# Performance work log

Hardware: AMD Instinct MI355X
Metric: run time of the kernel (lower is better)

Reference implementation:

```python
import jax, jax.numpy as jnp
import numpy as np
from jax import lax

IMAGE_SIZE = 224
BLUR_SIGMA = 4.0   # PIL GaussianBlur(radius=4) ~ sigma 4
BLUR_RADIUS = 8    # kernel support = 2*radius+1 = 17


def _gaussian_blur(img):
    # img: [1,1,H,W]; separable gaussian applied as a single 2D depthwise conv
    x = jnp.arange(-BLUR_RADIUS, BLUR_RADIUS + 1, dtype=img.dtype)
    k1 = jnp.exp(-0.5 * (x / BLUR_SIGMA) ** 2)
    k1 = k1 / k1.sum()
    k2 = jnp.outer(k1, k1)[None, None]  # [1,1,K,K]
    pad = jnp.pad(img, ((0, 0), (0, 0), (BLUR_RADIUS, BLUR_RADIUS), (BLUR_RADIUS, BLUR_RADIUS)), mode='reflect')
    return lax.conv_general_dilated(pad, k2, (1, 1), 'VALID',
                                    dimension_numbers=('NCHW', 'OIHW', 'NCHW'))


def _level_map(lib, fmap, idx):
    # lib: [N,C,H,W], fmap: [1,C,H,W], idx: [k]
    nearest = lib[idx]                                     # gather -> [k,C,H,W]
    d = jnp.sqrt(jnp.sum((nearest - fmap) ** 2, axis=1))   # L2 over channels -> [k,H,W]
    smin = jnp.min(d, axis=0)                              # min over k neighbors -> [H,W]
    # bilinear upsample (half-pixel centers == torch align_corners=False)
    up = jax.image.resize(smin, (IMAGE_SIZE, IMAGE_SIZE), method='bilinear')
    return up[None, None]                                  # [1,1,224,224]


def reference(z, z_lib, fmap0, fmap1, fmap2, lib0, lib1, lib2, k):
    # image-level kNN score
    dist = jnp.sqrt(jnp.sum((z_lib - z[None, :]) ** 2, axis=1))  # [N]
    neg_vals, idx = lax.top_k(-dist, k)                          # k smallest distances
    z_score = jnp.mean(-neg_vals)
    # pixel-level anomaly map: per-level min distance over the k nearest images
    s_map = (_level_map(lib0, fmap0, idx)
             + _level_map(lib1, fmap1, idx)
             + _level_map(lib2, fmap2, idx))
    return (z_score, _gaussian_blur(s_map))


def setup_inputs() -> dict:
    key = jax.random.key(0)
    ks = jax.random.split(key, 8)
    N = 128
    return {
        'z': jax.random.normal(ks[0], (1024,), dtype=jnp.float32),
        'z_lib': jax.random.normal(ks[1], (N, 1024), dtype=jnp.float32),
        'fmap0': jax.random.normal(ks[2], (1, 256, 56, 56), dtype=jnp.float32),
        'fmap1': jax.random.normal(ks[3], (1, 512, 28, 28), dtype=jnp.float32),
        'fmap2': jax.random.normal(ks[4], (1, 1024, 14, 14), dtype=jnp.float32),
        'lib0': jax.random.normal(ks[5], (N, 256, 56, 56), dtype=jnp.float32),
        'lib1': jax.random.normal(ks[6], (N, 512, 28, 28), dtype=jnp.float32),
        'lib2': jax.random.normal(ks[7], (N, 1024, 14, 14), dtype=jnp.float32),
        'k': 50,
    }
```

## Files before the change

kernel.cpp:

```cpp
#include <hip/hip_runtime.h>
#include <math.h>

#define NLIB 128
#define INFBITS 0x7F800000u

typedef float f32x4 __attribute__((ext_vector_type(4)));

static __device__ __forceinline__ int iclamp(int v, int lo, int hi) {
    return v < lo ? lo : (v > hi ? hi : v);
}

__global__ __launch_bounds__(256)
void row_dist_kernel(const float* __restrict__ z, const float* __restrict__ z_lib,
                     float* __restrict__ dist2) {
    const int n = blockIdx.x;
    const int tid = threadIdx.x, wave = tid >> 6, lane = tid & 63;
    const f32x4 a = ((const f32x4*)(z_lib + (size_t)n * 1024))[tid];
    const f32x4 b = ((const f32x4*)z)[tid];
    f32x4 d = a - b;
    f32x4 s = d * d;
    float acc = s[0] + s[1] + s[2] + s[3];
    for (int off = 32; off > 0; off >>= 1) acc += __shfl_down(acc, off, 64);
    __shared__ float ws4[4];
    if (lane == 0) ws4[wave] = acc;
    __syncthreads();
    if (tid == 0) dist2[n] = ws4[0] + ws4[1] + ws4[2] + ws4[3];
}

__global__ __launch_bounds__(128)
void select_kernel(const float* __restrict__ dist2, const int* __restrict__ kp,
                   float* __restrict__ zscore, int* __restrict__ idx,
                   unsigned* __restrict__ sb0, unsigned* __restrict__ sb1,
                   unsigned* __restrict__ sb2) {
    __shared__ float d[NLIB];
    __shared__ float contrib[NLIB];
    const int tid = threadIdx.x;
    d[tid] = dist2[tid];
    for (int i = tid; i < 3136; i += 128) sb0[i] = INFBITS;
    for (int i = tid; i < 784;  i += 128) sb1[i] = INFBITS;
    for (int i = tid; i < 196;  i += 128) sb2[i] = INFBITS;
    __syncthreads();
    const int k = *kp;
    const float dd = d[tid];
    int rank = 0;
#pragma unroll 8
    for (int m = 0; m < NLIB; ++m) {
        const float dm = d[m];
        rank += (dm < dd || (dm == dd && m < tid)) ? 1 : 0;
    }
    if (rank < k) idx[rank] = tid;
    contrib[tid] = (rank < k) ? sqrtf(dd) : 0.f;
    __syncthreads();
    if (tid == 0) {
        float s = 0.f;
        for (int m = 0; m < NLIB; ++m) s += contrib[m];
        zscore[0] = s / (float)k;
    }
}

template <int C, int NQ, int QT>
static __device__ __forceinline__ void dist_min_level(const float* __restrict__ lib,
                                                      const float* __restrict__ fmap,
                                                      int img, int qt,
                                                      unsigned* __restrict__ sb,
                                                      f32x4* __restrict__ part) {
    constexpr int G  = 256 / QT;
    constexpr int CW = C / G;
    const int tid = threadIdx.x;
    const int ql  = tid & (QT - 1);
    const int g   = tid / QT;
    const int q   = qt * QT + ql;
    const int qc  = q < NQ ? q : NQ - 1;
    const f32x4* __restrict__ lp = (const f32x4*)lib + ((size_t)img * C + g * CW) * NQ + qc;
    const f32x4* __restrict__ fp = (const f32x4*)fmap + ((size_t)g * CW) * NQ + qc;
    f32x4 acc = {};
#pragma unroll 8
    for (int c = 0; c < CW; ++c) {
        f32x4 a = lp[(size_t)c * NQ];
        f32x4 f = fp[(size_t)c * NQ];
        f32x4 d = a - f;
        acc += d * d;
    }
    part[tid] = acc;
    __syncthreads();
    if (tid < QT && q < NQ) {
        f32x4 s = part[tid];
#pragma unroll
        for (int gg = 1; gg < G; ++gg) s += part[gg * QT + tid];
        atomicMin(sb + q * 4 + 0, __float_as_uint(s[0]));
        atomicMin(sb + q * 4 + 1, __float_as_uint(s[1]));
        atomicMin(sb + q * 4 + 2, __float_as_uint(s[2]));
        atomicMin(sb + q * 4 + 3, __float_as_uint(s[3]));
    }
}

__global__ __launch_bounds__(256)
void dist_min_kernel(const float* __restrict__ lib0, const float* __restrict__ fmap0,
                     const float* __restrict__ lib1, const float* __restrict__ fmap1,
                     const float* __restrict__ lib2, const float* __restrict__ fmap2,
                     const int* __restrict__ kp, const int* __restrict__ idx,
                     unsigned* __restrict__ sb0, unsigned* __restrict__ sb1,
                     unsigned* __restrict__ sb2) {
    __shared__ f32x4 part[256];
    const int n = blockIdx.y;
    if (n >= *kp) return;
    const int t = blockIdx.x;
    const int img = idx[n];
    if (t < 13)      dist_min_level<256, 784, 64>(lib0, fmap0, img, t, sb0, part);
    else if (t < 20) dist_min_level<512, 196, 32>(lib1, fmap1, img, t - 13, sb1, part);
    else             dist_min_level<1024, 49, 16>(lib2, fmap2, img, t - 20, sb2, part);
}

static __device__ __forceinline__ void samp(int o, float inv_f, int sz, int& i0, int& i1,
                                            float& fr) {
    float c  = (o + 0.5f) * inv_f - 0.5f;
    float fl = floorf(c);
    fr = c - fl;
    int i = (int)fl;
    i0 = iclamp(i, 0, sz - 1);
    i1 = iclamp(i + 1, 0, sz - 1);
}

static __device__ __forceinline__ float ldsq(const unsigned* __restrict__ sb, int w, int y, int x) {
    return sqrtf(__uint_as_float(sb[y * w + x]));
}

static __device__ __forceinline__ float bilerp_sq(const unsigned* __restrict__ sb, int w,
                                                  int y0, int y1, int x0, int x1,
                                                  float fy, float fx) {
    float a = ldsq(sb, w, y0, x0), b = ldsq(sb, w, y0, x1);
    float c = ldsq(sb, w, y1, x0), d = ldsq(sb, w, y1, x1);
    float top = a + (b - a) * fx;
    float bot = c + (d - c) * fx;
    return top + (bot - top) * fy;
}

static __device__ __forceinline__ int reflect224(int i) {
    if (i < 0) i = -i;
    if (i > 223) i = 446 - i;
    return i;
}

static __device__ __forceinline__ void gauss_w(float* w) {
    float tot = 0.f;
#pragma unroll
    for (int j = 0; j < 17; ++j) {
        float t = (j - 8) * 0.25f;
        w[j] = expf(-0.5f * t * t);
        tot += w[j];
    }
    float inv = 1.f / tot;
#pragma unroll
    for (int j = 0; j < 17; ++j) w[j] *= inv;
}

__global__ __launch_bounds__(256)
void up_blurh_kernel(const unsigned* __restrict__ sb0, const unsigned* __restrict__ sb1,
                     const unsigned* __restrict__ sb2, float* __restrict__ tmp) {
    __shared__ float row[224];
    const int y = blockIdx.x, x = threadIdx.x;
    int y0, y1, x0, x1; float fy, fx;
    if (x < 224) {
        float v = 0.f;
        samp(y, 0.25f, 56, y0, y1, fy);   samp(x, 0.25f, 56, x0, x1, fx);
        v += bilerp_sq(sb0, 56, y0, y1, x0, x1, fy, fx);
        samp(y, 0.125f, 28, y0, y1, fy);  samp(x, 0.125f, 28, x0, x1, fx);
        v += bilerp_sq(sb1, 28, y0, y1, x0, x1, fy, fx);
        samp(y, 0.0625f, 14, y0, y1, fy); samp(x, 0.0625f, 14, x0, x1, fx);
        v += bilerp_sq(sb2, 14, y0, y1, x0, x1, fy, fx);
        row[x] = v;
    }
    __syncthreads();
    if (x < 224) {
        float w[17];
        gauss_w(w);
        float acc = 0.f;
#pragma unroll
        for (int j = 0; j < 17; ++j) acc += w[j] * row[reflect224(x + j - 8)];
        tmp[y * 224 + x] = acc;
    }
}

__global__ __launch_bounds__(256)
void blur_v_kernel(const float* __restrict__ in, float* __restrict__ out) {
    const int i = blockIdx.x * blockDim.x + threadIdx.x;
    if (i >= 224 * 224) return;
    const int y = i / 224, x = i % 224;
    float w[17];
    gauss_w(w);
    float acc = 0.f;
#pragma unroll
    for (int j = 0; j < 17; ++j) acc += w[j] * in[reflect224(y + j - 8) * 224 + x];
    out[i] = acc;
}

extern "C" void kernel_launch(void* const* d_in, const int* in_sizes, int n_in,
                              void* d_out, int out_size, void* d_ws, size_t ws_size,
                              hipStream_t stream) {
    const float* z     = (const float*)d_in[0];
    const float* z_lib = (const float*)d_in[1];
    const float* fmap0 = (const float*)d_in[2];
    const float* fmap1 = (const float*)d_in[3];
    const float* fmap2 = (const float*)d_in[4];
    const float* lib0  = (const float*)d_in[5];
    const float* lib1  = (const float*)d_in[6];
    const float* lib2  = (const float*)d_in[7];
    const int*   kp    = (const int*)d_in[8];
    float* out = (float*)d_out;

    constexpr size_t OFF_IDX   = 0;
    constexpr size_t OFF_DIST2 = 1024;
    constexpr size_t OFF_SB0   = 2048;
    constexpr size_t OFF_SB1   = 16384;
    constexpr size_t OFF_SB2   = 20480;
    constexpr size_t OFF_TMP   = 24576;

    char* ws = (char*)d_ws;
    int*      idx   = (int*)(ws + OFF_IDX);
    float*    dist2 = (float*)(ws + OFF_DIST2);
    unsigned* sb0   = (unsigned*)(ws + OFF_SB0);
    unsigned* sb1   = (unsigned*)(ws + OFF_SB1);
    unsigned* sb2   = (unsigned*)(ws + OFF_SB2);
    float*    tmp   = (float*)(ws + OFF_TMP);

    row_dist_kernel<<<dim3(NLIB), dim3(256), 0, stream>>>(z, z_lib, dist2);
    select_kernel<<<dim3(1), dim3(128), 0, stream>>>(dist2, kp, out, idx, sb0, sb1, sb2);
    dist_min_kernel<<<dim3(24, NLIB), dim3(256), 0, stream>>>(
        lib0, fmap0, lib1, fmap1, lib2, fmap2, kp, idx, sb0, sb1, sb2);
    up_blurh_kernel<<<dim3(224), dim3(256), 0, stream>>>(sb0, sb1, sb2, tmp);
    blur_v_kernel<<<dim3(196), dim3(256), 0, stream>>>(tmp, out + 1);
}
```

Before: 82.40 us.

## Process two images per block, fuse upsample and blur, fold init

```diff
diff --git a/kernel.cpp b/kernel.cpp
--- a/kernel.cpp
+++ b/kernel.cpp
@@ -12,9 +12,15 @@
 
 __global__ __launch_bounds__(256)
 void row_dist_kernel(const float* __restrict__ z, const float* __restrict__ z_lib,
-                     float* __restrict__ dist2) {
+                     float* __restrict__ dist2, unsigned* __restrict__ sb0,
+                     unsigned* __restrict__ sb1, unsigned* __restrict__ sb2) {
     const int n = blockIdx.x;
     const int tid = threadIdx.x, wave = tid >> 6, lane = tid & 63;
+    const int gid = n * 256 + tid;
+    if (gid < 3136)      sb0[gid] = INFBITS;
+    else if (gid < 3920) sb1[gid - 3136] = INFBITS;
+    else if (gid < 4116) sb2[gid - 3920] = INFBITS;
+
     const f32x4 a = ((const f32x4*)(z_lib + (size_t)n * 1024))[tid];
     const f32x4 b = ((const f32x4*)z)[tid];
     f32x4 d = a - b;
@@ -29,16 +35,11 @@
 
 __global__ __launch_bounds__(128)
 void select_kernel(const float* __restrict__ dist2, const int* __restrict__ kp,
-                   float* __restrict__ zscore, int* __restrict__ idx,
-                   unsigned* __restrict__ sb0, unsigned* __restrict__ sb1,
-                   unsigned* __restrict__ sb2) {
+                   float* __restrict__ zscore, int* __restrict__ idx) {
     __shared__ float d[NLIB];
     __shared__ float contrib[NLIB];
     const int tid = threadIdx.x;
     d[tid] = dist2[tid];
-    for (int i = tid; i < 3136; i += 128) sb0[i] = INFBITS;
-    for (int i = tid; i < 784;  i += 128) sb1[i] = INFBITS;
-    for (int i = tid; i < 196;  i += 128) sb2[i] = INFBITS;
     __syncthreads();
     const int k = *kp;
     const float dd = d[tid];
@@ -61,9 +62,10 @@
 template <int C, int NQ, int QT>
 static __device__ __forceinline__ void dist_min_level(const float* __restrict__ lib,
                                                       const float* __restrict__ fmap,
-                                                      int img, int qt,
+                                                      int img0, int img1, int qt,
                                                       unsigned* __restrict__ sb,
-                                                      f32x4* __restrict__ part) {
+                                                      f32x4* __restrict__ partA,
+                                                      f32x4* __restrict__ partB) {
     constexpr int G  = 256 / QT;
     constexpr int CW = C / G;
     const int tid = threadIdx.x;
@@ -71,26 +73,39 @@
     const int g   = tid / QT;
     const int q   = qt * QT + ql;
     const int qc  = q < NQ ? q : NQ - 1;
-    const f32x4* __restrict__ lp = (const f32x4*)lib + ((size_t)img * C + g * CW) * NQ + qc;
-    const f32x4* __restrict__ fp = (const f32x4*)fmap + ((size_t)g * CW) * NQ + qc;
-    f32x4 acc = {};
-#pragma unroll 8
+    const f32x4* __restrict__ lp0 = (const f32x4*)lib + ((size_t)img0 * C + g * CW) * NQ + qc;
+    const f32x4* __restrict__ lp1 = (const f32x4*)lib + ((size_t)img1 * C + g * CW) * NQ + qc;
+    const f32x4* __restrict__ fp  = (const f32x4*)fmap + ((size_t)g * CW) * NQ + qc;
+    f32x4 acc0 = {}, acc1 = {};
+#pragma unroll 4
     for (int c = 0; c < CW; ++c) {
-        f32x4 a = lp[(size_t)c * NQ];
-        f32x4 f = fp[(size_t)c * NQ];
-        f32x4 d = a - f;
-        acc += d * d;
-    }
-    part[tid] = acc;
+        f32x4 f  = fp[(size_t)c * NQ];
+        f32x4 a0 = __builtin_nontemporal_load(lp0 + (size_t)c * NQ);
+        f32x4 a1 = __builtin_nontemporal_load(lp1 + (size_t)c * NQ);
+        f32x4 d0 = a0 - f;
+        f32x4 d1 = a1 - f;
+        acc0 += d0 * d0;
+        acc1 += d1 * d1;
+    }
+    partA[tid] = acc0;
+    partB[tid] = acc1;
     __syncthreads();
     if (tid < QT && q < NQ) {
-        f32x4 s = part[tid];
-#pragma unroll
-        for (int gg = 1; gg < G; ++gg) s += part[gg * QT + tid];
-        atomicMin(sb + q * 4 + 0, __float_as_uint(s[0]));
-        atomicMin(sb + q * 4 + 1, __float_as_uint(s[1]));
-        atomicMin(sb + q * 4 + 2, __float_as_uint(s[2]));
-        atomicMin(sb + q * 4 + 3, __float_as_uint(s[3]));
+        f32x4 s0 = partA[tid];
+        f32x4 s1 = partB[tid];
+#pragma unroll
+        for (int gg = 1; gg < G; ++gg) {
+            s0 += partA[gg * QT + tid];
+            s1 += partB[gg * QT + tid];
+        }
+        atomicMin(sb + q * 4 + 0, __float_as_uint(s0[0]));
+        atomicMin(sb + q * 4 + 1, __float_as_uint(s0[1]));
+        atomicMin(sb + q * 4 + 2, __float_as_uint(s0[2]));
+        atomicMin(sb + q * 4 + 3, __float_as_uint(s0[3]));
+        atomicMin(sb + q * 4 + 0, __float_as_uint(s1[0]));
+        atomicMin(sb + q * 4 + 1, __float_as_uint(s1[1]));
+        atomicMin(sb + q * 4 + 2, __float_as_uint(s1[2]));
+        atomicMin(sb + q * 4 + 3, __float_as_uint(s1[3]));
     }
 }
 
@@ -101,14 +116,17 @@
                      const int* __restrict__ kp, const int* __restrict__ idx,
                      unsigned* __restrict__ sb0, unsigned* __restrict__ sb1,
                      unsigned* __restrict__ sb2) {
-    __shared__ f32x4 part[256];
-    const int n = blockIdx.y;
-    if (n >= *kp) return;
+    __shared__ f32x4 partA[256];
+    __shared__ f32x4 partB[256];
+    const int k = *kp;
+    const int n0 = blockIdx.y * 2;
+    if (n0 >= k) return;
+    const int n1 = (n0 + 1 < k) ? n0 + 1 : k - 1;
     const int t = blockIdx.x;
-    const int img = idx[n];
-    if (t < 13)      dist_min_level<256, 784, 64>(lib0, fmap0, img, t, sb0, part);
-    else if (t < 20) dist_min_level<512, 196, 32>(lib1, fmap1, img, t - 13, sb1, part);
-    else             dist_min_level<1024, 49, 16>(lib2, fmap2, img, t - 20, sb2, part);
+    const int img0 = idx[n0], img1 = idx[n1];
+    if (t < 13)      dist_min_level<256, 784, 64>(lib0, fmap0, img0, img1, t, sb0, partA, partB);
+    else if (t < 20) dist_min_level<512, 196, 32>(lib1, fmap1, img0, img1, t - 13, sb1, partA, partB);
+    else             dist_min_level<1024, 49, 16>(lib2, fmap2, img0, img1, t - 20, sb2, partA, partB);
 }
 
 static __device__ __forceinline__ void samp(int o, float inv_f, int sz, int& i0, int& i1,
@@ -155,43 +173,47 @@
 }
 
 __global__ __launch_bounds__(256)
-void up_blurh_kernel(const unsigned* __restrict__ sb0, const unsigned* __restrict__ sb1,
-                     const unsigned* __restrict__ sb2, float* __restrict__ tmp) {
-    __shared__ float row[224];
-    const int y = blockIdx.x, x = threadIdx.x;
-    int y0, y1, x0, x1; float fy, fx;
-    if (x < 224) {
-        float v = 0.f;
-        samp(y, 0.25f, 56, y0, y1, fy);   samp(x, 0.25f, 56, x0, x1, fx);
-        v += bilerp_sq(sb0, 56, y0, y1, x0, x1, fy, fx);
-        samp(y, 0.125f, 28, y0, y1, fy);  samp(x, 0.125f, 28, x0, x1, fx);
-        v += bilerp_sq(sb1, 28, y0, y1, x0, x1, fy, fx);
-        samp(y, 0.0625f, 14, y0, y1, fy); samp(x, 0.0625f, 14, x0, x1, fx);
-        v += bilerp_sq(sb2, 14, y0, y1, x0, x1, fy, fx);
-        row[x] = v;
-    }
-    __syncthreads();
-    if (x < 224) {
-        float w[17];
-        gauss_w(w);
-        float acc = 0.f;
-#pragma unroll
-        for (int j = 0; j < 17; ++j) acc += w[j] * row[reflect224(x + j - 8)];
-        tmp[y * 224 + x] = acc;
-    }
-}
-
-__global__ __launch_bounds__(256)
-void blur_v_kernel(const float* __restrict__ in, float* __restrict__ out) {
-    const int i = blockIdx.x * blockDim.x + threadIdx.x;
-    if (i >= 224 * 224) return;
-    const int y = i / 224, x = i % 224;
+void up_blur_kernel(const unsigned* __restrict__ sb0, const unsigned* __restrict__ sb1,
+                    const unsigned* __restrict__ sb2, float* __restrict__ outmap) {
+    __shared__ float sm[32][224];
+    __shared__ float hb[32][224];
+    const int y0 = blockIdx.x * 16;
+    const int tid = threadIdx.x;
     float w[17];
     gauss_w(w);
-    float acc = 0.f;
-#pragma unroll
-    for (int j = 0; j < 17; ++j) acc += w[j] * in[reflect224(y + j - 8) * 224 + x];
-    out[i] = acc;
+
+    for (int i = tid; i < 32 * 224; i += 256) {
+        const int r = i / 224, x = i - r * 224;
+        const int gy = reflect224(y0 - 8 + r);
+        int yy0, yy1, xx0, xx1; float fy, fx;
+        float v = 0.f;
+        samp(gy, 0.25f, 56, yy0, yy1, fy);   samp(x, 0.25f, 56, xx0, xx1, fx);
+        v += bilerp_sq(sb0, 56, yy0, yy1, xx0, xx1, fy, fx);
+        samp(gy, 0.125f, 28, yy0, yy1, fy);  samp(x, 0.125f, 28, xx0, xx1, fx);
+        v += bilerp_sq(sb1, 28, yy0, yy1, xx0, xx1, fy, fx);
+        samp(gy, 0.0625f, 14, yy0, yy1, fy); samp(x, 0.0625f, 14, xx0, xx1, fx);
+        v += bilerp_sq(sb2, 14, yy0, yy1, xx0, xx1, fy, fx);
+        sm[r][x] = v;
+    }
+    __syncthreads();
+
+    for (int i = tid; i < 32 * 224; i += 256) {
+        const int r = i / 224, x = i - r * 224;
+        float acc = 0.f;
+#pragma unroll
+        for (int j = 0; j < 17; ++j) acc += w[j] * sm[r][reflect224(x + j - 8)];
+        hb[r][x] = acc;
+    }
+    __syncthreads();
+
+    for (int i = tid; i < 16 * 224; i += 256) {
+        const int ry = i / 224, x = i - ry * 224;
+        const int y = y0 + ry;
+        float acc = 0.f;
+#pragma unroll
+        for (int j = 0; j < 17; ++j) acc += w[j] * hb[y + j - 8 - (y0 - 8)][x];
+        outmap[y * 224 + x] = acc;
+    }
 }
 
 extern "C" void kernel_launch(void* const* d_in, const int* in_sizes, int n_in,
@@ -213,7 +235,6 @@
     constexpr size_t OFF_SB0   = 2048;
     constexpr size_t OFF_SB1   = 16384;
     constexpr size_t OFF_SB2   = 20480;
-    constexpr size_t OFF_TMP   = 24576;
 
     char* ws = (char*)d_ws;
     int*      idx   = (int*)(ws + OFF_IDX);
@@ -221,12 +242,10 @@
     unsigned* sb0   = (unsigned*)(ws + OFF_SB0);
     unsigned* sb1   = (unsigned*)(ws + OFF_SB1);
     unsigned* sb2   = (unsigned*)(ws + OFF_SB2);
-    float*    tmp   = (float*)(ws + OFF_TMP);
-
-    row_dist_kernel<<<dim3(NLIB), dim3(256), 0, stream>>>(z, z_lib, dist2);
-    select_kernel<<<dim3(1), dim3(128), 0, stream>>>(dist2, kp, out, idx, sb0, sb1, sb2);
-    dist_min_kernel<<<dim3(24, NLIB), dim3(256), 0, stream>>>(
+
+    row_dist_kernel<<<dim3(NLIB), dim3(256), 0, stream>>>(z, z_lib, dist2, sb0, sb1, sb2);
+    select_kernel<<<dim3(1), dim3(128), 0, stream>>>(dist2, kp, out, idx);
+    dist_min_kernel<<<dim3(24, 64), dim3(256), 0, stream>>>(
         lib0, fmap0, lib1, fmap1, lib2, fmap2, kp, idx, sb0, sb1, sb2);
-    up_blurh_kernel<<<dim3(224), dim3(256), 0, stream>>>(sb0, sb1, sb2, tmp);
-    blur_v_kernel<<<dim3(196), dim3(256), 0, stream>>>(tmp, out + 1);
-}
+    up_blur_kernel<<<dim3(14), dim3(256), 0, stream>>>(sb0, sb1, sb2, out + 1);
+}
```

Result: slower. 111.9 us (+35.9%).

## Process four neighbor images per block to reuse fmap loads and cut atomics

Applied to the files above, without the earlier changes.

```diff
diff --git a/kernel.cpp b/kernel.cpp
--- a/kernel.cpp
+++ b/kernel.cpp
@@ -12,9 +12,15 @@
 
 __global__ __launch_bounds__(256)
 void row_dist_kernel(const float* __restrict__ z, const float* __restrict__ z_lib,
-                     float* __restrict__ dist2) {
+                     float* __restrict__ dist2, unsigned* __restrict__ sb0,
+                     unsigned* __restrict__ sb1, unsigned* __restrict__ sb2) {
     const int n = blockIdx.x;
     const int tid = threadIdx.x, wave = tid >> 6, lane = tid & 63;
+    const int gid = n * 256 + tid;
+    if (gid < 3136)      sb0[gid] = INFBITS;
+    else if (gid < 3920) sb1[gid - 3136] = INFBITS;
+    else if (gid < 4116) sb2[gid - 3920] = INFBITS;
+
     const f32x4 a = ((const f32x4*)(z_lib + (size_t)n * 1024))[tid];
     const f32x4 b = ((const f32x4*)z)[tid];
     f32x4 d = a - b;
@@ -29,16 +35,11 @@
 
 __global__ __launch_bounds__(128)
 void select_kernel(const float* __restrict__ dist2, const int* __restrict__ kp,
-                   float* __restrict__ zscore, int* __restrict__ idx,
-                   unsigned* __restrict__ sb0, unsigned* __restrict__ sb1,
-                   unsigned* __restrict__ sb2) {
+                   float* __restrict__ zscore, int* __restrict__ idx) {
     __shared__ float d[NLIB];
     __shared__ float contrib[NLIB];
     const int tid = threadIdx.x;
     d[tid] = dist2[tid];
-    for (int i = tid; i < 3136; i += 128) sb0[i] = INFBITS;
-    for (int i = tid; i < 784;  i += 128) sb1[i] = INFBITS;
-    for (int i = tid; i < 196;  i += 128) sb2[i] = INFBITS;
     __syncthreads();
     const int k = *kp;
     const float dd = d[tid];
@@ -61,9 +62,9 @@
 template <int C, int NQ, int QT>
 static __device__ __forceinline__ void dist_min_level(const float* __restrict__ lib,
                                                       const float* __restrict__ fmap,
-                                                      int img, int qt,
-                                                      unsigned* __restrict__ sb,
-                                                      f32x4* __restrict__ part) {
+                                                      const int* __restrict__ img,
+                                                      int qt, unsigned* __restrict__ sb,
+                                                      f32x4 (* __restrict__ part)[256]) {
     constexpr int G  = 256 / QT;
     constexpr int CW = C / G;
     const int tid = threadIdx.x;
@@ -71,26 +72,49 @@
     const int g   = tid / QT;
     const int q   = qt * QT + ql;
     const int qc  = q < NQ ? q : NQ - 1;
-    const f32x4* __restrict__ lp = (const f32x4*)lib + ((size_t)img * C + g * CW) * NQ + qc;
     const f32x4* __restrict__ fp = (const f32x4*)fmap + ((size_t)g * CW) * NQ + qc;
-    f32x4 acc = {};
-#pragma unroll 8
-    for (int c = 0; c < CW; ++c) {
-        f32x4 a = lp[(size_t)c * NQ];
-        f32x4 f = fp[(size_t)c * NQ];
-        f32x4 d = a - f;
-        acc += d * d;
-    }
-    part[tid] = acc;
+    const f32x4* lp[4];
+#pragma unroll
+    for (int j = 0; j < 4; ++j)
+        lp[j] = (const f32x4*)lib + ((size_t)img[j] * C + g * CW) * NQ + qc;
+
+    f32x4 acc0 = {}, acc1 = {}, acc2 = {}, acc3 = {};
+#pragma unroll
+    for (int cc = 0; cc < CW / 8; ++cc) {
+        f32x4 f[8];
+#pragma unroll
+        for (int u = 0; u < 8; ++u) f[u] = fp[(size_t)(cc * 8 + u) * NQ];
+#pragma unroll
+        for (int u = 0; u < 8; ++u) {
+            const size_t off = (size_t)(cc * 8 + u) * NQ;
+            f32x4 d0 = lp[0][off] - f[u]; acc0 += d0 * d0;
+            f32x4 d1 = lp[1][off] - f[u]; acc1 += d1 * d1;
+            f32x4 d2 = lp[2][off] - f[u]; acc2 += d2 * d2;
+            f32x4 d3 = lp[3][off] - f[u]; acc3 += d3 * d3;
+        }
+    }
+    part[0][tid] = acc0;
+    part[1][tid] = acc1;
+    part[2][tid] = acc2;
+    part[3][tid] = acc3;
     __syncthreads();
     if (tid < QT && q < NQ) {
-        f32x4 s = part[tid];
-#pragma unroll
-        for (int gg = 1; gg < G; ++gg) s += part[gg * QT + tid];
-        atomicMin(sb + q * 4 + 0, __float_as_uint(s[0]));
-        atomicMin(sb + q * 4 + 1, __float_as_uint(s[1]));
-        atomicMin(sb + q * 4 + 2, __float_as_uint(s[2]));
-        atomicMin(sb + q * 4 + 3, __float_as_uint(s[3]));
+        f32x4 s0 = part[0][tid], s1 = part[1][tid], s2 = part[2][tid], s3 = part[3][tid];
+#pragma unroll
+        for (int gg = 1; gg < G; ++gg) {
+            s0 += part[0][gg * QT + tid];
+            s1 += part[1][gg * QT + tid];
+            s2 += part[2][gg * QT + tid];
+            s3 += part[3][gg * QT + tid];
+        }
+        f32x4 m;
+#pragma unroll
+        for (int e = 0; e < 4; ++e)
+            m[e] = fminf(fminf(s0[e], s1[e]), fminf(s2[e], s3[e]));
+        atomicMin(sb + q * 4 + 0, __float_as_uint(m[0]));
+        atomicMin(sb + q * 4 + 1, __float_as_uint(m[1]));
+        atomicMin(sb + q * 4 + 2, __float_as_uint(m[2]));
+        atomicMin(sb + q * 4 + 3, __float_as_uint(m[3]));
     }
 }
 
@@ -101,11 +125,18 @@
                      const int* __restrict__ kp, const int* __restrict__ idx,
                      unsigned* __restrict__ sb0, unsigned* __restrict__ sb1,
                      unsigned* __restrict__ sb2) {
-    __shared__ f32x4 part[256];
-    const int n = blockIdx.y;
-    if (n >= *kp) return;
+    __shared__ f32x4 part[4][256];
+    const int k = *kp;
+    const int nb = blockIdx.y * 4;
+    if (nb >= k) return;
+    int img[4];
+#pragma unroll
+    for (int j = 0; j < 4; ++j) {
+        int n = nb + j;
+        n = n < k ? n : k - 1;
+        img[j] = idx[n];
+    }
     const int t = blockIdx.x;
-    const int img = idx[n];
     if (t < 13)      dist_min_level<256, 784, 64>(lib0, fmap0, img, t, sb0, part);
     else if (t < 20) dist_min_level<512, 196, 32>(lib1, fmap1, img, t - 13, sb1, part);
     else             dist_min_level<1024, 49, 16>(lib2, fmap2, img, t - 20, sb2, part);
@@ -223,9 +254,9 @@
     unsigned* sb2   = (unsigned*)(ws + OFF_SB2);
     float*    tmp   = (float*)(ws + OFF_TMP);
 
-    row_dist_kernel<<<dim3(NLIB), dim3(256), 0, stream>>>(z, z_lib, dist2);
-    select_kernel<<<dim3(1), dim3(128), 0, stream>>>(dist2, kp, out, idx, sb0, sb1, sb2);
-    dist_min_kernel<<<dim3(24, NLIB), dim3(256), 0, stream>>>(
+    row_dist_kernel<<<dim3(NLIB), dim3(256), 0, stream>>>(z, z_lib, dist2, sb0, sb1, sb2);
+    select_kernel<<<dim3(1), dim3(128), 0, stream>>>(dist2, kp, out, idx);
+    dist_min_kernel<<<dim3(24, 32), dim3(256), 0, stream>>>(
         lib0, fmap0, lib1, fmap1, lib2, fmap2, kp, idx, sb0, sb1, sb2);
     up_blurh_kernel<<<dim3(224), dim3(256), 0, stream>>>(sb0, sb1, sb2, tmp);
     blur_v_kernel<<<dim3(196), dim3(256), 0, stream>>>(tmp, out + 1);
```

After: 149.0 us. 80.9% more time.

## Fuse top-k selection into distance-min kernel and double its grid

Applied to the files above, without the earlier changes.

```diff
diff --git a/kernel.cpp b/kernel.cpp
--- a/kernel.cpp
+++ b/kernel.cpp
@@ -12,9 +12,15 @@
 
 __global__ __launch_bounds__(256)
 void row_dist_kernel(const float* __restrict__ z, const float* __restrict__ z_lib,
-                     float* __restrict__ dist2) {
+                     float* __restrict__ dist2, unsigned* __restrict__ sb0,
+                     unsigned* __restrict__ sb1, unsigned* __restrict__ sb2) {
     const int n = blockIdx.x;
     const int tid = threadIdx.x, wave = tid >> 6, lane = tid & 63;
+    const int gid = n * 256 + tid;
+    if (gid < 3136)      sb0[gid] = INFBITS;
+    else if (gid < 3920) sb1[gid - 3136] = INFBITS;
+    else if (gid < 4116) sb2[gid - 3920] = INFBITS;
+
     const f32x4 a = ((const f32x4*)(z_lib + (size_t)n * 1024))[tid];
     const f32x4 b = ((const f32x4*)z)[tid];
     f32x4 d = a - b;
@@ -25,37 +31,6 @@
     if (lane == 0) ws4[wave] = acc;
     __syncthreads();
     if (tid == 0) dist2[n] = ws4[0] + ws4[1] + ws4[2] + ws4[3];
-}
-
-__global__ __launch_bounds__(128)
-void select_kernel(const float* __restrict__ dist2, const int* __restrict__ kp,
-                   float* __restrict__ zscore, int* __restrict__ idx,
-                   unsigned* __restrict__ sb0, unsigned* __restrict__ sb1,
-                   unsigned* __restrict__ sb2) {
-    __shared__ float d[NLIB];
-    __shared__ float contrib[NLIB];
-    const int tid = threadIdx.x;
-    d[tid] = dist2[tid];
-    for (int i = tid; i < 3136; i += 128) sb0[i] = INFBITS;
-    for (int i = tid; i < 784;  i += 128) sb1[i] = INFBITS;
-    for (int i = tid; i < 196;  i += 128) sb2[i] = INFBITS;
-    __syncthreads();
-    const int k = *kp;
-    const float dd = d[tid];
-    int rank = 0;
-#pragma unroll 8
-    for (int m = 0; m < NLIB; ++m) {
-        const float dm = d[m];
-        rank += (dm < dd || (dm == dd && m < tid)) ? 1 : 0;
-    }
-    if (rank < k) idx[rank] = tid;
-    contrib[tid] = (rank < k) ? sqrtf(dd) : 0.f;
-    __syncthreads();
-    if (tid == 0) {
-        float s = 0.f;
-        for (int m = 0; m < NLIB; ++m) s += contrib[m];
-        zscore[0] = s / (float)k;
-    }
 }
 
 template <int C, int NQ, int QT>
@@ -98,17 +73,44 @@
 void dist_min_kernel(const float* __restrict__ lib0, const float* __restrict__ fmap0,
                      const float* __restrict__ lib1, const float* __restrict__ fmap1,
                      const float* __restrict__ lib2, const float* __restrict__ fmap2,
-                     const int* __restrict__ kp, const int* __restrict__ idx,
+                     const int* __restrict__ kp, const float* __restrict__ dist2,
+                     float* __restrict__ zscore,
                      unsigned* __restrict__ sb0, unsigned* __restrict__ sb1,
                      unsigned* __restrict__ sb2) {
     __shared__ f32x4 part[256];
+    __shared__ float dsh[NLIB];
+    __shared__ float contrib[NLIB];
+    __shared__ int img_sh;
+    const int k = *kp;
     const int n = blockIdx.y;
-    if (n >= *kp) return;
+    if (n >= k) return;
+    const int tid = threadIdx.x;
     const int t = blockIdx.x;
-    const int img = idx[n];
-    if (t < 13)      dist_min_level<256, 784, 64>(lib0, fmap0, img, t, sb0, part);
-    else if (t < 20) dist_min_level<512, 196, 32>(lib1, fmap1, img, t - 13, sb1, part);
-    else             dist_min_level<1024, 49, 16>(lib2, fmap2, img, t - 20, sb2, part);
+
+    if (tid < NLIB) dsh[tid] = dist2[tid];
+    __syncthreads();
+    if (tid < NLIB) {
+        const float dd = dsh[tid];
+        int rank = 0;
+#pragma unroll 8
+        for (int m = 0; m < NLIB; ++m) {
+            const float dm = dsh[m];
+            rank += (dm < dd || (dm == dd && m < tid)) ? 1 : 0;
+        }
+        if (rank == n) img_sh = tid;
+        if (t == 0 && n == 0) contrib[tid] = (rank < k) ? sqrtf(dd) : 0.f;
+    }
+    __syncthreads();
+    if (t == 0 && n == 0 && tid == 0) {
+        float s = 0.f;
+        for (int m = 0; m < NLIB; ++m) s += contrib[m];
+        zscore[0] = s / (float)k;
+    }
+    const int img = img_sh;
+
+    if (t < 26)      dist_min_level<256, 784, 32>(lib0, fmap0, img, t, sb0, part);
+    else if (t < 40) dist_min_level<512, 196, 16>(lib1, fmap1, img, t - 26, sb1, part);
+    else             dist_min_level<1024, 49, 8>(lib2, fmap2, img, t - 40, sb2, part);
 }
 
 static __device__ __forceinline__ void samp(int o, float inv_f, int sz, int& i0, int& i1,
@@ -208,7 +210,6 @@
     const int*   kp    = (const int*)d_in[8];
     float* out = (float*)d_out;
 
-    constexpr size_t OFF_IDX   = 0;
     constexpr size_t OFF_DIST2 = 1024;
     constexpr size_t OFF_SB0   = 2048;
     constexpr size_t OFF_SB1   = 16384;
@@ -216,17 +217,15 @@
     constexpr size_t OFF_TMP   = 24576;
 
     char* ws = (char*)d_ws;
-    int*      idx   = (int*)(ws + OFF_IDX);
     float*    dist2 = (float*)(ws + OFF_DIST2);
     unsigned* sb0   = (unsigned*)(ws + OFF_SB0);
     unsigned* sb1   = (unsigned*)(ws + OFF_SB1);
     unsigned* sb2   = (unsigned*)(ws + OFF_SB2);
     float*    tmp   = (float*)(ws + OFF_TMP);
 
-    row_dist_kernel<<<dim3(NLIB), dim3(256), 0, stream>>>(z, z_lib, dist2);
-    select_kernel<<<dim3(1), dim3(128), 0, stream>>>(dist2, kp, out, idx, sb0, sb1, sb2);
-    dist_min_kernel<<<dim3(24, NLIB), dim3(256), 0, stream>>>(
-        lib0, fmap0, lib1, fmap1, lib2, fmap2, kp, idx, sb0, sb1, sb2);
+    row_dist_kernel<<<dim3(NLIB), dim3(256), 0, stream>>>(z, z_lib, dist2, sb0, sb1, sb2);
+    dist_min_kernel<<<dim3(48, NLIB), dim3(256), 0, stream>>>(
+        lib0, fmap0, lib1, fmap1, lib2, fmap2, kp, dist2, out, sb0, sb1, sb2);
     up_blurh_kernel<<<dim3(224), dim3(256), 0, stream>>>(sb0, sb1, sb2, tmp);
     blur_v_kernel<<<dim3(196), dim3(256), 0, stream>>>(tmp, out + 1);
 }
```

Measured after the change: 83.40 us. No clear change (+1.2%).
